# Performance work log

Hardware: AMD Instinct MI355X
Metric: run time of the kernel (lower is better)

## Reference

```python
import jax, jax.numpy as jnp
import numpy as np

N_NODES = 100000
N_EDGES = 1600000
HIDDEN = 64
NUM_GRAPHS = 512


def setup_inputs() -> dict:
    key = jax.random.key(0)
    k1, k2, k3, k4, k5, k6 = jax.random.split(key, 6)
    x = jax.random.normal(k1, (N_NODES, HIDDEN), dtype=jnp.float32)
    edge_index = jax.random.randint(k2, (2, N_EDGES), 0, N_NODES, dtype=jnp.int64)
    batch = jnp.sort(jax.random.randint(k3, (N_NODES,), 0, NUM_GRAPHS, dtype=jnp.int64))
    # SAGPooling's internal GraphConv(64 -> 1): lin_rel (with bias) on aggregated
    # neighbor features, lin_root (no bias) on self features.
    s = 1.0 / np.sqrt(HIDDEN)
    W_rel = jax.random.uniform(k4, (HIDDEN, 1), dtype=jnp.float32, minval=-s, maxval=s)
    b_rel = jax.random.uniform(k5, (1,), dtype=jnp.float32, minval=-s, maxval=s)
    W_root = jax.random.uniform(k6, (HIDDEN, 1), dtype=jnp.float32, minval=-s, maxval=s)
    return {"x": x, "edge_index": edge_index, "batch": batch,
            "W_rel": W_rel, "b_rel": b_rel, "W_root": W_root}


def reference(x, edge_index, batch, W_rel, b_rel, W_root):
    n = x.shape[0]
    src, dst = edge_index[0], edge_index[1]
    # GraphConv (aggr='add'): sum x_j over in-edges, then lin_rel(aggr)+lin_root(x)
    aggr = jax.ops.segment_sum(x[src], dst, num_segments=n)          # [N, H]
    score = (aggr @ W_rel + b_rel + x @ W_root)[:, 0]                # [N]
    # min_score=-1 -> scores softmax-normalized per graph; all nodes kept in order
    m = jax.ops.segment_max(score, batch, num_segments=NUM_GRAPHS)   # [G]
    e = jnp.exp(score - m[batch])
    z = jax.ops.segment_sum(e, batch, num_segments=NUM_GRAPHS)       # [G]
    att = e / z[batch]                                               # [N]
    att_x = x * att[:, None]                                         # [N, H]
    # global_add_pool
    return jax.ops.segment_sum(att_x, batch, num_segments=NUM_GRAPHS)  # [G, H]
```

## Files before the change

kernel.cpp:

```cpp
#include <hip/hip_runtime.h>
#include <math.h>
#include <stdint.h>


#define H 64
#define TILE 4096
#define NTHR_S 512
#define EPT (TILE / NTHR_S)
#define BUCKET_SZ 256
#define MAX_NB 400
#define CAP 5120
#define ROWS_PER_WAVE 64
#define PSCALE 16384.0f
#define INV_PSCALE 6.103515625e-05f

__global__ __launch_bounds__(256) void node_prep(
    const float4* __restrict__ x4, const float* __restrict__ W_rel,
    const float* __restrict__ W_root,
    float* __restrict__ p, float* __restrict__ r,
    float* __restrict__ num, float* __restrict__ z,
    unsigned int* __restrict__ cursor,
    int n_nodes, int num_elems, int n_graphs, int nb)
{
    int gid = (int)(blockIdx.x * blockDim.x + threadIdx.x);
    if (gid < num_elems) num[gid] = 0.0f;
    else if (gid < num_elems + n_graphs) z[gid - num_elems] = 0.0f;
    else if (gid < num_elems + n_graphs + nb)
        cursor[gid - num_elems - n_graphs] =
            (unsigned int)(gid - num_elems - n_graphs) * CAP;

    int node = blockIdx.x * 64 + (threadIdx.x >> 2);
    int q    = threadIdx.x & 3;
    if (node >= n_nodes) return;

    float pv = 0.0f, rv = 0.0f;
    #pragma unroll
    for (int kk = 0; kk < 4; ++kk) {
        float4 v = x4[node * 16 + kk * 4 + q];
        int c0 = (kk * 4 + q) * 4;
        pv += v.x * W_rel[c0] + v.y * W_rel[c0 + 1]
            + v.z * W_rel[c0 + 2] + v.w * W_rel[c0 + 3];
        rv += v.x * W_root[c0] + v.y * W_root[c0 + 1]
            + v.z * W_root[c0 + 2] + v.w * W_root[c0 + 3];
    }
    pv += __shfl_xor(pv, 1, 64); pv += __shfl_xor(pv, 2, 64);
    rv += __shfl_xor(rv, 1, 64); rv += __shfl_xor(rv, 2, 64);
    if (q == 0) { p[node] = pv; r[node] = rv; }
}

__global__ __launch_bounds__(NTHR_S) void edge_sort(
    const int* __restrict__ src, const int* __restrict__ dst,
    const float* __restrict__ p,
    unsigned int* __restrict__ cursor, unsigned int* __restrict__ sorted_g,
    int n_edges, int nb)
{
    __shared__ unsigned int hist[MAX_NB];
    __shared__ unsigned int gbase[MAX_NB];

    int b = blockIdx.x;
    int base = b * TILE;
    int tile_n = min(TILE, n_edges - base);
    int tid = threadIdx.x;

    if (tid < nb) hist[tid] = 0;
    __syncthreads();

    unsigned int dd[EPT]; int ss[EPT];
    float pv[EPT];
    unsigned int bk[EPT], pk[EPT], slot[EPT];

    #pragma unroll
    for (int u = 0; u < EPT; ++u) {
        int j = tid + u * NTHR_S;
        if (j < tile_n) { dd[u] = (unsigned int)dst[base + j];
                          ss[u] = src[base + j]; }
        else dd[u] = 0xFFFFFFFFu;
    }
    #pragma unroll
    for (int u = 0; u < EPT; ++u)
        if (dd[u] != 0xFFFFFFFFu) pv[u] = p[ss[u]];
    #pragma unroll
    for (int u = 0; u < EPT; ++u) {
        if (dd[u] != 0xFFFFFFFFu) {
            bk[u] = dd[u] >> 8;
            int q = (int)__float2int_rn(pv[u] * PSCALE);
            q = max(-8388607, min(8388607, q));
            pk[u] = ((unsigned int)q << 8) | (dd[u] & 255u);
            slot[u] = atomicAdd(&hist[bk[u]], 1u);
        }
    }
    __syncthreads();

    if (tid < nb) {
        unsigned int c = hist[tid];
        gbase[tid] = c ? atomicAdd(&cursor[tid], c) : 0u;
    }
    __syncthreads();

    #pragma unroll
    for (int u = 0; u < EPT; ++u) {
        if (dd[u] != 0xFFFFFFFFu) {
            unsigned int gi = gbase[bk[u]] + slot[u];
            if (gi < (bk[u] + 1) * (unsigned int)CAP)
                sorted_g[gi] = pk[u];
        }
    }
}

__global__ __launch_bounds__(256) void bucket_accum(
    const unsigned int* __restrict__ sorted_g,
    const unsigned int* __restrict__ cursor,
    const float* __restrict__ r,
    float* __restrict__ e_buf, int n_nodes)
{
    __shared__ int acc[BUCKET_SZ];
    int k = blockIdx.x;
    int tid = threadIdx.x;
    acc[tid] = 0;
    __syncthreads();

    unsigned int beg = (unsigned int)k * CAP;
    unsigned int cnt = min(cursor[k] - beg, (unsigned int)CAP);
    unsigned int n4  = cnt & ~3u;
    for (unsigned int j = tid * 4; j < n4; j += 1024) {
        uint4 v = *(const uint4*)(sorted_g + beg + j);
        atomicAdd(&acc[v.x & 255u], (int)v.x >> 8);
        atomicAdd(&acc[v.y & 255u], (int)v.y >> 8);
        atomicAdd(&acc[v.z & 255u], (int)v.z >> 8);
        atomicAdd(&acc[v.w & 255u], (int)v.w >> 8);
    }
    for (unsigned int j = n4 + tid; j < cnt; j += 256) {
        unsigned int v = sorted_g[beg + j];
        atomicAdd(&acc[v & 255u], (int)v >> 8);
    }
    __syncthreads();

    int node = k * BUCKET_SZ + tid;
    if (node < n_nodes)
        e_buf[node] = __expf((float)acc[tid] * INV_PSCALE + r[node]);
}

__global__ __launch_bounds__(256) void pool(
    const float* __restrict__ x, const float* __restrict__ e_buf,
    const int* __restrict__ batch,
    float* __restrict__ num, float* __restrict__ z, int n_nodes)
{
    int wid = threadIdx.x >> 6, lane = threadIdx.x & 63;
    int row0 = (blockIdx.x * 4 + wid) * ROWS_PER_WAVE;
    if (row0 >= n_nodes) return;
    int rend = min(row0 + ROWS_PER_WAVE, n_nodes);

    int cur_g = batch[row0];
    float acc = 0.0f, acce = 0.0f;
    for (int i = row0; i < rend; ++i) {
        int g = batch[i];
        if (g != cur_g) {
            unsafeAtomicAdd(&num[cur_g * H + lane], acc);
            if (lane == 0) unsafeAtomicAdd(&z[cur_g], acce);
            acc = 0.0f; acce = 0.0f;
            cur_g = g;
        }
        float e = e_buf[i];
        acc += x[i * H + lane] * e;
        acce += e;
    }
    unsafeAtomicAdd(&num[cur_g * H + lane], acc);
    if (lane == 0) unsafeAtomicAdd(&z[cur_g], acce);
}

__global__ __launch_bounds__(256) void finalize(
    const float* __restrict__ num, const float* __restrict__ z,
    float* __restrict__ out, int num_elems)
{
    int i = (int)(blockIdx.x * blockDim.x + threadIdx.x);
    if (i >= num_elems) return;
    float zz = z[i >> 6];
    out[i] = (zz != 0.0f) ? num[i] / zz : 0.0f;
}

extern "C" void kernel_launch(void* const* d_in, const int* in_sizes, int n_in,
                              void* d_out, int out_size, void* d_ws, size_t ws_size,
                              hipStream_t stream)
{
    const float* x      = (const float*)d_in[0];
    const int*   eidx   = (const int*)d_in[1];
    const int*   batch  = (const int*)d_in[2];
    const float* W_rel  = (const float*)d_in[3];
    const float* W_root = (const float*)d_in[5];
    float* out = (float*)d_out;

    const int n_nodes  = in_sizes[0] / H;
    const int n_edges  = in_sizes[1] / 2;
    const int n_graphs = out_size / H;
    const int nb     = (n_nodes + BUCKET_SZ - 1) / BUCKET_SZ;
    const int ntiles = (n_edges + TILE - 1) / TILE;

    const int* src = eidx;
    const int* dst = eidx + n_edges;

    float* p     = (float*)d_ws;
    float* r     = p + n_nodes;
    float* e_buf = r + n_nodes;
    float* z     = e_buf + n_nodes;
    float* num   = z + n_graphs;
    unsigned int* cursor = (unsigned int*)(num + out_size);
    uintptr_t raw = (uintptr_t)(cursor + nb);
    unsigned int* sorted_g = (unsigned int*)((raw + 15) & ~(uintptr_t)15);

    int np_blocks = (n_nodes + 63) / 64;
    node_prep<<<np_blocks, 256, 0, stream>>>(
        (const float4*)x, W_rel, W_root, p, r, num, z, cursor,
        n_nodes, out_size, n_graphs, nb);
    edge_sort<<<ntiles, NTHR_S, 0, stream>>>(src, dst, p, cursor, sorted_g,
                                             n_edges, nb);
    bucket_accum<<<nb, 256, 0, stream>>>(sorted_g, cursor, r, e_buf, n_nodes);
    pool<<<(n_nodes + 4 * ROWS_PER_WAVE - 1) / (4 * ROWS_PER_WAVE), 256, 0, stream>>>(
        x, e_buf, batch, num, z, n_nodes);
    finalize<<<(out_size + 255) / 256, 256, 0, stream>>>(num, z, out, out_size);
}
```

Before: 134.5 us.

## Stage edge scatter in LDS by bucket and add fast single-graph pool path

edge_sort now computes a block-wide prefix sum over bucket histograms, places the packed edges grouped by bucket in shared memory, and then writes them out in tile order so global stores to each bucket's region are contiguous. This replaces scattered global writes with more coalesced ones, at the cost of extra LDS (about 24KB more) and a multi-step scan with many barriers. The pool kernel halves rows per wave and adds an unrolled fast path when every row in a wave's chunk belongs to the same graph, which skips the per-row batch loads and branches.

```diff
diff --git a/kernel.cpp b/kernel.cpp
--- a/kernel.cpp
+++ b/kernel.cpp
@@ -10,7 +10,7 @@
 #define BUCKET_SZ 256
 #define MAX_NB 400
 #define CAP 5120
-#define ROWS_PER_WAVE 64
+#define ROWS_PER_WAVE 32
 #define PSCALE 16384.0f
 #define INV_PSCALE 6.103515625e-05f
 
@@ -55,7 +55,11 @@
     int n_edges, int nb)
 {
     __shared__ unsigned int hist[MAX_NB];
+    __shared__ unsigned int offs[MAX_NB];
     __shared__ unsigned int gbase[MAX_NB];
+    __shared__ unsigned int tsum[NTHR_S];
+    __shared__ unsigned int svals[TILE];
+    __shared__ unsigned short sbid[TILE];
 
     int b = blockIdx.x;
     int base = b * TILE;
@@ -91,19 +95,36 @@
     }
     __syncthreads();
 
+    unsigned int myv = (tid < nb) ? hist[tid] : 0;
+    tsum[tid] = myv;
+    __syncthreads();
+    for (int d1 = 1; d1 < NTHR_S; d1 <<= 1) {
+        unsigned int t2 = (tid >= d1) ? tsum[tid - d1] : 0;
+        __syncthreads();
+        tsum[tid] += t2;
+        __syncthreads();
+    }
     if (tid < nb) {
-        unsigned int c = hist[tid];
-        gbase[tid] = c ? atomicAdd(&cursor[tid], c) : 0u;
+        offs[tid] = tsum[tid] - myv;
+        gbase[tid] = myv ? atomicAdd(&cursor[tid], myv) : 0u;
     }
     __syncthreads();
 
     #pragma unroll
     for (int u = 0; u < EPT; ++u) {
         if (dd[u] != 0xFFFFFFFFu) {
-            unsigned int gi = gbase[bk[u]] + slot[u];
-            if (gi < (bk[u] + 1) * (unsigned int)CAP)
-                sorted_g[gi] = pk[u];
-        }
+            unsigned int pos = offs[bk[u]] + slot[u];
+            svals[pos] = pk[u];
+            sbid[pos]  = (unsigned short)bk[u];
+        }
+    }
+    __syncthreads();
+
+    for (int j = tid; j < tile_n; j += NTHR_S) {
+        unsigned int bb = sbid[j];
+        unsigned int gi = gbase[bb] + ((unsigned int)j - offs[bb]);
+        if (gi < (bb + 1) * (unsigned int)CAP)
+            sorted_g[gi] = svals[j];
     }
 }
 
@@ -150,7 +171,24 @@
     if (row0 >= n_nodes) return;
     int rend = min(row0 + ROWS_PER_WAVE, n_nodes);
 
-    int cur_g = batch[row0];
+    int g_first = batch[row0];
+    int g_last  = batch[rend - 1];
+
+    if (g_first == g_last && rend - row0 == ROWS_PER_WAVE) {
+        float acc = 0.0f, acce = 0.0f;
+        #pragma unroll 8
+        for (int u = 0; u < ROWS_PER_WAVE; ++u) {
+            int i = row0 + u;
+            float e = e_buf[i];
+            acc  += x[i * H + lane] * e;
+            acce += e;
+        }
+        unsafeAtomicAdd(&num[g_first * H + lane], acc);
+        if (lane == 0) unsafeAtomicAdd(&z[g_first], acce);
+        return;
+    }
+
+    int cur_g = g_first;
     float acc = 0.0f, acce = 0.0f;
     for (int i = row0; i < rend; ++i) {
         int g = batch[i];
@@ -161,7 +199,7 @@
             cur_g = g;
         }
         float e = e_buf[i];
-        acc += x[i * H + lane] * e;
+        acc  += x[i * H + lane] * e;
         acce += e;
     }
     unsafeAtomicAdd(&num[cur_g * H + lane], acc);
```

Result: faster. 126.6 us (-5.9%).
